# Kernel tuning notes

Hardware: AMD Instinct MI355X
Metric: run time of the kernel (lower is better)

## Reference

```python
import jax, jax.numpy as jnp
import numpy as np

N, E, D = 20000, 320000, 256
H, C = 8, 32  # heads, per-head channels (out_channels // heads)


def setup_inputs() -> dict:
    key = jax.random.key(0)
    ks = jax.random.split(key, 12)
    s = 1.0 / np.sqrt(D)
    return {
        "x": jax.random.normal(ks[0], (N, D), jnp.float32),
        "edge_index": jax.random.randint(ks[1], (2, E), 0, N, jnp.int64),
        "edge_attr": jax.random.normal(ks[2], (E, D), jnp.float32),
        "Wq": jax.random.normal(ks[3], (D, H * C), jnp.float32) * s,
        "bq": jnp.zeros((H * C,), jnp.float32),
        "Wk": jax.random.normal(ks[4], (D, H * C), jnp.float32) * s,
        "bk": jnp.zeros((H * C,), jnp.float32),
        "Wv": jax.random.normal(ks[5], (D, H * C), jnp.float32) * s,
        "bv": jnp.zeros((H * C,), jnp.float32),
        "We": jax.random.normal(ks[6], (D, H * C), jnp.float32) * s,  # lin_edge, no bias
        "Ws": jax.random.normal(ks[7], (D, H * C), jnp.float32) * s,  # lin_skip (root weight)
        "bs": jnp.zeros((H * C,), jnp.float32),
    }


def reference(x, edge_index, edge_attr, Wq, bq, Wk, bk, Wv, bv, We, Ws, bs):
    n = x.shape[0]
    src, dst = edge_index[0], edge_index[1]  # j (source), i (target)
    q = (x @ Wq + bq).reshape(n, H, C)
    k = (x @ Wk + bk).reshape(n, H, C)
    v = (x @ Wv + bv).reshape(n, H, C)
    e = (edge_attr @ We).reshape(-1, H, C)  # (E, H, C)

    kj = k[src] + e                      # key of source node + edge embedding
    alpha = jnp.einsum('ehc,ehc->eh', q[dst], kj) / jnp.sqrt(jnp.float32(C))
    # numerically-stable segment softmax over destination neighborhoods
    amax = jax.ops.segment_max(alpha, dst, num_segments=n)      # (N, H)
    ea = jnp.exp(alpha - amax[dst])                             # (E, H)
    denom = jax.ops.segment_sum(ea, dst, num_segments=n)        # (N, H)
    alpha = ea / (denom[dst] + 1e-16)

    msg = (v[src] + e) * alpha[:, :, None]                      # (E, H, C)
    out = jax.ops.segment_sum(msg, dst, num_segments=n)         # (N, H, C)
    out = out.reshape(n, H * C) + (x @ Ws + bs)                 # concat heads + skip
    return out
```

## Files before the change

### kernel.cpp

```cpp
#include <hip/hip_runtime.h>
#include <hip/hip_fp16.h>

#define N_NODES 20000
#define N_EDGES 320000
#define DIM 256

typedef _Float16 f16;
typedef unsigned int u32;
typedef f16 f16x8 __attribute__((ext_vector_type(8)));
typedef f16 f16x4 __attribute__((ext_vector_type(4)));
typedef float f32x4 __attribute__((ext_vector_type(4)));

#define GLL16(gsrc, ldst) __builtin_amdgcn_global_load_lds( \
    (const u32 __attribute__((address_space(1)))*)(gsrc),   \
    (u32 __attribute__((address_space(3)))*)(ldst), 16, 0, 0)

__global__ void prep_all(const float* __restrict__ Wq, const float* __restrict__ Wk,
                         const float* __restrict__ Wv, const float* __restrict__ Ws,
                         const float* __restrict__ We,
                         const float* __restrict__ bq, const float* __restrict__ bk,
                         const float* __restrict__ bv, const float* __restrict__ bs,
                         f16* __restrict__ wtbase, float* __restrict__ biasAll) {
    if (blockIdx.x < 1280) {
        int gid = blockIdx.x * 256 + threadIdx.x;
        int w = gid >> 16;
        int idx = gid & 65535;
        int k = idx >> 8, n = idx & 255;
        const float* W = (w == 0) ? Wq : (w == 1) ? Wk : (w == 2) ? Wv : (w == 3) ? Ws : We;
        wtbase[w * 65536 + n * 256 + k] = (f16)W[k * 256 + n];
    } else {
        int i = (blockIdx.x - 1280) * 256 + threadIdx.x;
        if (i < 1024) {
            int y = i >> 8, col = i & 255;
            const float* b = (y == 0) ? bq : (y == 1) ? bk : (y == 2) ? bv : bs;
            biasAll[i] = b[col];
        }
    }
}

template<int EDGE>
__global__ __launch_bounds__(256, 2) void gemm_v2(
    const float* __restrict__ A, const f16* __restrict__ WTbase,
    const float* __restrict__ biasAll,
    f16* __restrict__ outF16, float* __restrict__ outF32, int M)
{
    __shared__ __align__(16) char ldsB[2][16384];
    const int tid = threadIdx.x;
    const int wave = tid >> 6, lane = tid & 63;
    const int l16 = lane & 15, lg = lane >> 4;
    const int rowBase = blockIdx.x * 64 + (wave & 1) * 32;
    const int colBase = (wave >> 1) * 128;
    const int y = EDGE ? 0 : blockIdx.y;
    const f16* __restrict__ WT = WTbase + (EDGE ? 4 * 65536 : y * 65536);

    auto STAGE = [&](int b, int ks) {
#pragma unroll
        for (int i = 0; i < 4; ++i) {
            const int r = wave * 4 + i;
            const int n = r * 16 + (lane >> 2);
            const int kc = lane & 3;
            const f16* src = WT + n * 256 + ks * 32 + kc * 8;
            GLL16(src, &ldsB[b][r * 1024]);
        }
    };

    f32x4 a_lo[2], a_hi[2];
    auto LOADA = [&](int ks) {
#pragma unroll
        for (int m = 0; m < 2; ++m) {
            int row = rowBase + m * 16 + l16;
            if (row >= M) row = M - 1;
            const float* ap = A + (size_t)row * DIM + ks * 32 + lg * 8;
            a_lo[m] = *(const f32x4*)ap;
            a_hi[m] = *(const f32x4*)(ap + 4);
        }
    };

    f32x4 acc[2][8];
#pragma unroll
    for (int m = 0; m < 2; ++m)
#pragma unroll
        for (int c = 0; c < 8; ++c) acc[m][c] = (f32x4){0.f, 0.f, 0.f, 0.f};

    STAGE(0, 0);
    LOADA(0);

#pragma unroll
    for (int ks = 0; ks < 8; ++ks) {
        __syncthreads();
        if (ks < 7) STAGE((ks + 1) & 1, ks + 1);
        f16x8 afr[2];
#pragma unroll
        for (int m = 0; m < 2; ++m) {
#pragma unroll
            for (int j = 0; j < 4; ++j) {
                afr[m][j]     = (f16)a_lo[m][j];
                afr[m][4 + j] = (f16)a_hi[m][j];
            }
        }
        if (ks < 7) LOADA(ks + 1);
        const char* bbuf = ldsB[ks & 1];
#pragma unroll
        for (int ct = 0; ct < 8; ++ct) {
            f16x8 b = *(const f16x8*)(bbuf + (colBase + ct * 16 + l16) * 64 + lg * 16);
            acc[0][ct] = __builtin_amdgcn_mfma_f32_16x16x32_f16(afr[0], b, acc[0][ct], 0, 0, 0);
            acc[1][ct] = __builtin_amdgcn_mfma_f32_16x16x32_f16(afr[1], b, acc[1][ct], 0, 0, 0);
        }
    }

#pragma unroll
    for (int m = 0; m < 2; ++m) {
#pragma unroll
        for (int ct = 0; ct < 8; ++ct) {
            const int col = colBase + ct * 16 + l16;
            const float bv = EDGE ? 0.f : biasAll[y * 256 + col];
#pragma unroll
            for (int i = 0; i < 4; ++i) {
                const int row = rowBase + m * 16 + lg * 4 + i;
                if (row < M) {
                    const float val = acc[m][ct][i] + bv;
                    if (EDGE) {
                        outF16[(size_t)row * 256 + col] = (f16)val;
                    } else if (y < 3) {
                        (outF16 + (size_t)y * N_NODES * 256)[(size_t)row * 256 + col] = (f16)val;
                    } else {
                        outF32[(size_t)row * 256 + col] = val;
                    }
                }
            }
        }
    }
}

__global__ void count_deg(const int* __restrict__ dst, int* __restrict__ deg) {
    int e = blockIdx.x * blockDim.x + threadIdx.x;
    if (e < N_EDGES) atomicAdd(&deg[dst[e]], 1);
}

__global__ __launch_bounds__(1024) void scan_deg(const int* __restrict__ deg,
                                                 int* __restrict__ rowptr,
                                                 int* __restrict__ cursor) {
    __shared__ int part[1024];
    const int t = threadIdx.x;
    const int CH = (N_NODES + 1023) / 1024;
    const int base = t * CH;
    int s = 0;
    for (int i = 0; i < CH; ++i) { int n = base + i; if (n < N_NODES) s += deg[n]; }
    part[t] = s;
    __syncthreads();
    for (int off = 1; off < 1024; off <<= 1) {
        int v = (t >= off) ? part[t - off] : 0;
        __syncthreads();
        part[t] += v;
        __syncthreads();
    }
    int run = (t == 0) ? 0 : part[t - 1];
    for (int i = 0; i < CH; ++i) {
        int n = base + i;
        if (n < N_NODES) { int dn = deg[n]; rowptr[n] = run; cursor[n] = run; run += dn; }
    }
    if (t == 1023) rowptr[N_NODES] = part[1023];
}

__global__ void scatter_edges(const int* __restrict__ dst, int* __restrict__ cursor,
                              int* __restrict__ eids) {
    int e = blockIdx.x * blockDim.x + threadIdx.x;
    if (e < N_EDGES) { int p = atomicAdd(&cursor[dst[e]], 1); eids[p] = e; }
}

__global__ __launch_bounds__(256) void aggregate(
    const f16* __restrict__ qf, const f16* __restrict__ kf, const f16* __restrict__ vf,
    const f16* __restrict__ ef, const int* __restrict__ srcArr,
    const int* __restrict__ rowptr, const int* __restrict__ eids,
    float* __restrict__ out)
{
    const int wave = threadIdx.x >> 6;
    const int lane = threadIdx.x & 63;
    const int node = blockIdx.x * 4 + wave;
    if (node >= N_NODES) return;
    const int c0 = lane * 4;

    f32x4 qv;
    {
        f16x4 qh = *(const f16x4*)(qf + (size_t)node * 256 + c0);
        qv = (f32x4){(float)qh[0], (float)qh[1], (float)qh[2], (float)qh[3]};
    }
    float acc0 = 0.f, acc1 = 0.f, acc2 = 0.f, acc3 = 0.f, den = 0.f;
    const int beg = rowptr[node], end = rowptr[node + 1];
    for (int idx = beg; idx < end; ++idx) {
        const int eid = eids[idx];
        const int src = srcArr[eid];
        f16x4 eh = *(const f16x4*)(ef + (size_t)eid * 256 + c0);
        f16x4 kh = *(const f16x4*)(kf + (size_t)src * 256 + c0);
        f16x4 vh = *(const f16x4*)(vf + (size_t)src * 256 + c0);
        const float e0 = (float)eh[0], e1 = (float)eh[1], e2 = (float)eh[2], e3 = (float)eh[3];
        float d = qv[0] * ((float)kh[0] + e0) + qv[1] * ((float)kh[1] + e1)
                + qv[2] * ((float)kh[2] + e2) + qv[3] * ((float)kh[3] + e3);
        d += __shfl_xor(d, 1);
        d += __shfl_xor(d, 2);
        d += __shfl_xor(d, 4);
        const float ea = __expf(d * 0.1767766952966369f);
        den += ea;
        acc0 += ea * ((float)vh[0] + e0);
        acc1 += ea * ((float)vh[1] + e1);
        acc2 += ea * ((float)vh[2] + e2);
        acc3 += ea * ((float)vh[3] + e3);
    }
    const float inv = 1.0f / (den + 1e-16f);
    const size_t ob = (size_t)node * 256 + c0;
    f32x4 o = *(f32x4*)(out + ob);
    o[0] += acc0 * inv; o[1] += acc1 * inv; o[2] += acc2 * inv; o[3] += acc3 * inv;
    *(f32x4*)(out + ob) = o;
}

extern "C" void kernel_launch(void* const* d_in, const int* in_sizes, int n_in,
                              void* d_out, int out_size, void* d_ws, size_t ws_size,
                              hipStream_t stream) {
    const float* x   = (const float*)d_in[0];
    const int*   ei  = (const int*)d_in[1];
    const float* ea  = (const float*)d_in[2];
    const float* Wq  = (const float*)d_in[3];
    const float* bq  = (const float*)d_in[4];
    const float* Wk  = (const float*)d_in[5];
    const float* bk  = (const float*)d_in[6];
    const float* Wv  = (const float*)d_in[7];
    const float* bv  = (const float*)d_in[8];
    const float* We  = (const float*)d_in[9];
    const float* Ws  = (const float*)d_in[10];
    const float* bs  = (const float*)d_in[11];
    float* out = (float*)d_out;

    const int* srcArr = ei;
    const int* dstArr = ei + N_EDGES;

    char* w = (char*)d_ws;
    size_t off = 0;
    f16* wtbase = (f16*)(w + off); off += 5 * 65536 * 2;
    f16* qf = (f16*)(w + off); off += (size_t)N_NODES * 256 * 2;
    f16* kf = (f16*)(w + off); off += (size_t)N_NODES * 256 * 2;
    f16* vf = (f16*)(w + off); off += (size_t)N_NODES * 256 * 2;
    f16* ef = (f16*)(w + off); off += (size_t)N_EDGES * 256 * 2;
    int* deg    = (int*)(w + off); off += 80016;
    int* rowptr = (int*)(w + off); off += 80016;
    int* cursor = (int*)(w + off); off += 80016;
    int* eids   = (int*)(w + off); off += (size_t)N_EDGES * 4;
    float* biasAll = (float*)(w + off); off += 4 * 256 * 4;
    (void)ws_size; (void)n_in; (void)in_sizes; (void)out_size;

    prep_all<<<1284, 256, 0, stream>>>(Wq, Wk, Wv, Ws, We, bq, bk, bv, bs, wtbase, biasAll);

    hipMemsetAsync(deg, 0, N_NODES * 4, stream);
    count_deg<<<(N_EDGES + 255) / 256, 256, 0, stream>>>(dstArr, deg);
    scan_deg<<<1, 1024, 0, stream>>>(deg, rowptr, cursor);
    scatter_edges<<<(N_EDGES + 255) / 256, 256, 0, stream>>>(dstArr, cursor, eids);

    dim3 gnode((N_NODES + 63) / 64, 4);
    gemm_v2<0><<<gnode, 256, 0, stream>>>(x, wtbase, biasAll, qf, out, N_NODES);
    gemm_v2<1><<<N_EDGES / 64, 256, 0, stream>>>(ea, wtbase, nullptr, ef, nullptr, N_EDGES);

    aggregate<<<N_NODES / 4, 256, 0, stream>>>(qf, kf, vf, ef, srcArr, rowptr, eids, out);
}
```

Baseline: 391.8 us.

## Stage full weight matrix in LDS with swizzle and deepen A prefetch in GEMM

The GEMM block grows from 256 to 512 threads covering 128 rows. The whole 256x256 f16 weight matrix (128 KB) is loaded into LDS once per block with an XOR swizzle, which removes the per-k-step double-buffer syncs. The A operand is now prefetched three k-steps ahead instead of one, and the degree memset is replaced by a small zeroing kernel. The trade-off is heavy LDS use (128 KB per block), which limits blocks per CU and puts the whole weight load up front before any compute.

```diff
diff --git a/kernel.cpp b/kernel.cpp
--- a/kernel.cpp
+++ b/kernel.cpp
@@ -38,75 +38,83 @@
     }
 }
 
+__global__ void zero_deg(int* __restrict__ deg) {
+    int i = blockIdx.x * 256 + threadIdx.x;
+    if (i < N_NODES) deg[i] = 0;
+}
+
 template<int EDGE>
-__global__ __launch_bounds__(256, 2) void gemm_v2(
+__global__ __launch_bounds__(512, 2) void gemm_v3(
     const float* __restrict__ A, const f16* __restrict__ WTbase,
     const float* __restrict__ biasAll,
     f16* __restrict__ outF16, float* __restrict__ outF32, int M)
 {
-    __shared__ __align__(16) char ldsB[2][16384];
+    __shared__ __align__(16) char ldsB[131072];
     const int tid = threadIdx.x;
     const int wave = tid >> 6, lane = tid & 63;
     const int l16 = lane & 15, lg = lane >> 4;
-    const int rowBase = blockIdx.x * 64 + (wave & 1) * 32;
-    const int colBase = (wave >> 1) * 128;
-    const int y = EDGE ? 0 : blockIdx.y;
-    const f16* __restrict__ WT = WTbase + (EDGE ? 4 * 65536 : y * 65536);
-
-    auto STAGE = [&](int b, int ks) {
-#pragma unroll
-        for (int i = 0; i < 4; ++i) {
-            const int r = wave * 4 + i;
-            const int n = r * 16 + (lane >> 2);
-            const int kc = lane & 3;
-            const f16* src = WT + n * 256 + ks * 32 + kc * 8;
-            GLL16(src, &ldsB[b][r * 1024]);
-        }
-    };
-
-    f32x4 a_lo[2], a_hi[2];
-    auto LOADA = [&](int ks) {
+    const int rowBase = blockIdx.x * 128 + (wave & 3) * 32;
+    const int colBase = (wave >> 2) * 128;
+    const int y = EDGE ? 4 : blockIdx.y;
+    const f16* __restrict__ WT = WTbase + y * 65536;
+
+    {
+        const int nrel = lane >> 2;
+        const int kc = (lane & 3) ^ ((lane >> 3) & 3);
+        const f16* srcBase = WT + wave * 32 + kc * 8;
+#pragma unroll
+        for (int r = 0; r < 16; ++r) {
+            const f16* src = srcBase + (size_t)(r * 16 + nrel) * 256;
+            GLL16(src, &ldsB[wave * 16384 + r * 1024]);
+        }
+    }
+
+    f32x4 alo[3][2], ahi[3][2];
+#define LOADA(ks_, s_) do {                                                   \
+    _Pragma("unroll")                                                         \
+    for (int m_ = 0; m_ < 2; ++m_) {                                          \
+        int row_ = rowBase + m_ * 16 + l16;                                   \
+        if (row_ >= M) row_ = M - 1;                                          \
+        const float* ap_ = A + (size_t)row_ * DIM + (ks_) * 32 + lg * 8;      \
+        alo[s_][m_] = *(const f32x4*)ap_;                                     \
+        ahi[s_][m_] = *(const f32x4*)(ap_ + 4);                               \
+    } } while (0)
+
+    LOADA(0, 0); LOADA(1, 1); LOADA(2, 2);
+
+    f32x4 acc[2][8];
+#pragma unroll
+    for (int m = 0; m < 2; ++m)
+#pragma unroll
+        for (int c = 0; c < 8; ++c) acc[m][c] = (f32x4){0.f, 0.f, 0.f, 0.f};
+
+    const int swzRead = (lg ^ ((l16 >> 1) & 3)) * 16;
+
+    __syncthreads();
+
+#pragma unroll
+    for (int ks = 0; ks < 8; ++ks) {
+        const int slot = ks % 3;
+        f16x8 afr[2];
 #pragma unroll
         for (int m = 0; m < 2; ++m) {
-            int row = rowBase + m * 16 + l16;
-            if (row >= M) row = M - 1;
-            const float* ap = A + (size_t)row * DIM + ks * 32 + lg * 8;
-            a_lo[m] = *(const f32x4*)ap;
-            a_hi[m] = *(const f32x4*)(ap + 4);
-        }
-    };
-
-    f32x4 acc[2][8];
-#pragma unroll
-    for (int m = 0; m < 2; ++m)
-#pragma unroll
-        for (int c = 0; c < 8; ++c) acc[m][c] = (f32x4){0.f, 0.f, 0.f, 0.f};
-
-    STAGE(0, 0);
-    LOADA(0);
-
-#pragma unroll
-    for (int ks = 0; ks < 8; ++ks) {
-        __syncthreads();
-        if (ks < 7) STAGE((ks + 1) & 1, ks + 1);
-        f16x8 afr[2];
-#pragma unroll
-        for (int m = 0; m < 2; ++m) {
 #pragma unroll
             for (int j = 0; j < 4; ++j) {
-                afr[m][j]     = (f16)a_lo[m][j];
-                afr[m][4 + j] = (f16)a_hi[m][j];
+                afr[m][j]     = (f16)alo[slot][m][j];
+                afr[m][4 + j] = (f16)ahi[slot][m][j];
             }
         }
-        if (ks < 7) LOADA(ks + 1);
-        const char* bbuf = ldsB[ks & 1];
+        if (ks < 5) LOADA(ks + 3, slot);
+        const char* bbuf = ldsB + ks * 16384;
 #pragma unroll
         for (int ct = 0; ct < 8; ++ct) {
-            f16x8 b = *(const f16x8*)(bbuf + (colBase + ct * 16 + l16) * 64 + lg * 16);
+            const int n = colBase + ct * 16 + l16;
+            f16x8 b = *(const f16x8*)(bbuf + n * 64 + swzRead);
             acc[0][ct] = __builtin_amdgcn_mfma_f32_16x16x32_f16(afr[0], b, acc[0][ct], 0, 0, 0);
             acc[1][ct] = __builtin_amdgcn_mfma_f32_16x16x32_f16(afr[1], b, acc[1][ct], 0, 0, 0);
         }
     }
+#undef LOADA
 
 #pragma unroll
     for (int m = 0; m < 2; ++m) {
@@ -249,14 +257,14 @@
 
     prep_all<<<1284, 256, 0, stream>>>(Wq, Wk, Wv, Ws, We, bq, bk, bv, bs, wtbase, biasAll);
 
-    hipMemsetAsync(deg, 0, N_NODES * 4, stream);
+    zero_deg<<<(N_NODES + 255) / 256, 256, 0, stream>>>(deg);
     count_deg<<<(N_EDGES + 255) / 256, 256, 0, stream>>>(dstArr, deg);
     scan_deg<<<1, 1024, 0, stream>>>(deg, rowptr, cursor);
     scatter_edges<<<(N_EDGES + 255) / 256, 256, 0, stream>>>(dstArr, cursor, eids);
 
-    dim3 gnode((N_NODES + 63) / 64, 4);
-    gemm_v2<0><<<gnode, 256, 0, stream>>>(x, wtbase, biasAll, qf, out, N_NODES);
-    gemm_v2<1><<<N_EDGES / 64, 256, 0, stream>>>(ea, wtbase, nullptr, ef, nullptr, N_EDGES);
+    dim3 gnode((N_NODES + 127) / 128, 4);
+    gemm_v3<0><<<gnode, 512, 0, stream>>>(x, wtbase, biasAll, qf, out, N_NODES);
+    gemm_v3<1><<<N_EDGES / 128, 512, 0, stream>>>(ea, wtbase, nullptr, ef, nullptr, N_EDGES);
 
     aggregate<<<N_NODES / 4, 256, 0, stream>>>(qf, kf, vf, ef, srcArr, rowptr, eids, out);
 }
```

Result: no change. 385.7 us (-1.5%).

## Write edge projections in CSR order and restructure GEMM with full-K LDS staging

Applied to the files above, without the earlier changes.

The edge GEMM now gathers edge_attr rows through the CSR permutation (eids), so edge embeddings are stored in destination-sorted order. The aggregate kernel can then read e and a pre-permuted src array contiguously instead of taking two dependent indirections per edge. The GEMM is rewritten to 512 threads with 128-row by 128-column tiles. It loads the whole K dimension of A into registers and a swizzled full-K B tile into LDS in one stage, which removes the per-k-step double-buffer syncs. Other changes: the deg memset is folded into prep_all, and the aggregate loop is unrolled by two. The cost is a random gather on edge_attr reads and higher register and LDS pressure in the GEMM.

```diff
diff --git a/kernel.cpp b/kernel.cpp
--- a/kernel.cpp
+++ b/kernel.cpp
@@ -20,7 +20,8 @@
                          const float* __restrict__ We,
                          const float* __restrict__ bq, const float* __restrict__ bk,
                          const float* __restrict__ bv, const float* __restrict__ bs,
-                         f16* __restrict__ wtbase, float* __restrict__ biasAll) {
+                         f16* __restrict__ wtbase, float* __restrict__ biasAll,
+                         int* __restrict__ deg) {
     if (blockIdx.x < 1280) {
         int gid = blockIdx.x * 256 + threadIdx.x;
         int w = gid >> 16;
@@ -28,104 +29,96 @@
         int k = idx >> 8, n = idx & 255;
         const float* W = (w == 0) ? Wq : (w == 1) ? Wk : (w == 2) ? Wv : (w == 3) ? Ws : We;
         wtbase[w * 65536 + n * 256 + k] = (f16)W[k * 256 + n];
+    } else if (blockIdx.x < 1284) {
+        int i = (blockIdx.x - 1280) * 256 + threadIdx.x;
+        int y = i >> 8, col = i & 255;
+        const float* b = (y == 0) ? bq : (y == 1) ? bk : (y == 2) ? bv : bs;
+        biasAll[i] = b[col];
     } else {
-        int i = (blockIdx.x - 1280) * 256 + threadIdx.x;
-        if (i < 1024) {
-            int y = i >> 8, col = i & 255;
-            const float* b = (y == 0) ? bq : (y == 1) ? bk : (y == 2) ? bv : bs;
-            biasAll[i] = b[col];
-        }
+        int i = (blockIdx.x - 1284) * 256 + threadIdx.x;
+        if (i < N_NODES) deg[i] = 0;
     }
 }
 
 template<int EDGE>
-__global__ __launch_bounds__(256, 2) void gemm_v2(
+__global__ __launch_bounds__(512, 4) void gemm_v4(
     const float* __restrict__ A, const f16* __restrict__ WTbase,
-    const float* __restrict__ biasAll,
+    const float* __restrict__ biasAll, const int* __restrict__ eids,
     f16* __restrict__ outF16, float* __restrict__ outF32, int M)
 {
-    __shared__ __align__(16) char ldsB[2][16384];
+    __shared__ __align__(16) char lds[65536];
     const int tid = threadIdx.x;
     const int wave = tid >> 6, lane = tid & 63;
     const int l16 = lane & 15, lg = lane >> 4;
-    const int rowBase = blockIdx.x * 64 + (wave & 1) * 32;
-    const int colBase = (wave >> 1) * 128;
-    const int y = EDGE ? 0 : blockIdx.y;
-    const f16* __restrict__ WT = WTbase + (EDGE ? 4 * 65536 : y * 65536);
-
-    auto STAGE = [&](int b, int ks) {
+    const int y = blockIdx.y;
+    const int outSel  = EDGE ? 4 : (y >> 1);
+    const int colHalf = EDGE ? y : (y & 1);
+    const f16* __restrict__ WT = WTbase + outSel * 65536 + colHalf * 128 * 256;
+    const int rowBase = blockIdx.x * 128 + wave * 16;
+
+    const int slot = rowBase + l16;
+    int arow;
+    if (EDGE) arow = eids[slot];
+    else      arow = (slot < M) ? slot : M - 1;
+    const float* ap = A + (size_t)arow * DIM;
+    f32x4 lo[8], hi[8];
+#pragma unroll
+    for (int ks = 0; ks < 8; ++ks) {
+        lo[ks] = *(const f32x4*)(ap + ks * 32 + lg * 8);
+        hi[ks] = *(const f32x4*)(ap + ks * 32 + lg * 8 + 4);
+    }
+
+    {
+        const int p = lane & 31;
+#pragma unroll
+        for (int r = 0; r < 8; ++r) {
+            const int nrel = wave * 16 + r * 2 + (lane >> 5);
+            const f16* src = WT + nrel * 256 + (p ^ (nrel & 31)) * 8;
+            GLL16(src, &lds[(wave * 16 + r * 2) * 512]);
+        }
+    }
+
+    f16x8 afr[8];
+#pragma unroll
+    for (int ks = 0; ks < 8; ++ks) {
+#pragma unroll
+        for (int j = 0; j < 4; ++j) {
+            afr[ks][j]     = (f16)lo[ks][j];
+            afr[ks][4 + j] = (f16)hi[ks][j];
+        }
+    }
+
+    f32x4 acc[8];
+#pragma unroll
+    for (int c = 0; c < 8; ++c) acc[c] = (f32x4){0.f, 0.f, 0.f, 0.f};
+
+    __syncthreads();
+
+#pragma unroll
+    for (int ks = 0; ks < 8; ++ks) {
+#pragma unroll
+        for (int ct = 0; ct < 8; ++ct) {
+            const int nrel = ct * 16 + l16;
+            f16x8 b = *(const f16x8*)(lds + nrel * 512 + (((ks * 4 + lg) ^ (nrel & 31)) * 16));
+            acc[ct] = __builtin_amdgcn_mfma_f32_16x16x32_f16(afr[ks], b, acc[ct], 0, 0, 0);
+        }
+    }
+
+#pragma unroll
+    for (int ct = 0; ct < 8; ++ct) {
+        const int col = colHalf * 128 + ct * 16 + l16;
+        const float bv = EDGE ? 0.f : biasAll[outSel * 256 + col];
 #pragma unroll
         for (int i = 0; i < 4; ++i) {
-            const int r = wave * 4 + i;
-            const int n = r * 16 + (lane >> 2);
-            const int kc = lane & 3;
-            const f16* src = WT + n * 256 + ks * 32 + kc * 8;
-            GLL16(src, &ldsB[b][r * 1024]);
-        }
-    };
-
-    f32x4 a_lo[2], a_hi[2];
-    auto LOADA = [&](int ks) {
-#pragma unroll
-        for (int m = 0; m < 2; ++m) {
-            int row = rowBase + m * 16 + l16;
-            if (row >= M) row = M - 1;
-            const float* ap = A + (size_t)row * DIM + ks * 32 + lg * 8;
-            a_lo[m] = *(const f32x4*)ap;
-            a_hi[m] = *(const f32x4*)(ap + 4);
-        }
-    };
-
-    f32x4 acc[2][8];
-#pragma unroll
-    for (int m = 0; m < 2; ++m)
-#pragma unroll
-        for (int c = 0; c < 8; ++c) acc[m][c] = (f32x4){0.f, 0.f, 0.f, 0.f};
-
-    STAGE(0, 0);
-    LOADA(0);
-
-#pragma unroll
-    for (int ks = 0; ks < 8; ++ks) {
-        __syncthreads();
-        if (ks < 7) STAGE((ks + 1) & 1, ks + 1);
-        f16x8 afr[2];
-#pragma unroll
-        for (int m = 0; m < 2; ++m) {
-#pragma unroll
-            for (int j = 0; j < 4; ++j) {
-                afr[m][j]     = (f16)a_lo[m][j];
-                afr[m][4 + j] = (f16)a_hi[m][j];
-            }
-        }
-        if (ks < 7) LOADA(ks + 1);
-        const char* bbuf = ldsB[ks & 1];
-#pragma unroll
-        for (int ct = 0; ct < 8; ++ct) {
-            f16x8 b = *(const f16x8*)(bbuf + (colBase + ct * 16 + l16) * 64 + lg * 16);
-            acc[0][ct] = __builtin_amdgcn_mfma_f32_16x16x32_f16(afr[0], b, acc[0][ct], 0, 0, 0);
-            acc[1][ct] = __builtin_amdgcn_mfma_f32_16x16x32_f16(afr[1], b, acc[1][ct], 0, 0, 0);
-        }
-    }
-
-#pragma unroll
-    for (int m = 0; m < 2; ++m) {
-#pragma unroll
-        for (int ct = 0; ct < 8; ++ct) {
-            const int col = colBase + ct * 16 + l16;
-            const float bv = EDGE ? 0.f : biasAll[y * 256 + col];
-#pragma unroll
-            for (int i = 0; i < 4; ++i) {
-                const int row = rowBase + m * 16 + lg * 4 + i;
-                if (row < M) {
-                    const float val = acc[m][ct][i] + bv;
-                    if (EDGE) {
-                        outF16[(size_t)row * 256 + col] = (f16)val;
-                    } else if (y < 3) {
-                        (outF16 + (size_t)y * N_NODES * 256)[(size_t)row * 256 + col] = (f16)val;
-                    } else {
-                        outF32[(size_t)row * 256 + col] = val;
-                    }
+            const int row = rowBase + lg * 4 + i;
+            if (EDGE || row < M) {
+                const float val = acc[ct][i] + bv;
+                if (EDGE) {
+                    outF16[(size_t)row * 256 + col] = (f16)val;
+                } else if (outSel < 3) {
+                    (outF16 + (size_t)outSel * N_NODES * 256)[(size_t)row * 256 + col] = (f16)val;
+                } else {
+                    outF32[(size_t)row * 256 + col] = val;
                 }
             }
         }
@@ -162,17 +155,21 @@
     if (t == 1023) rowptr[N_NODES] = part[1023];
 }
 
-__global__ void scatter_edges(const int* __restrict__ dst, int* __restrict__ cursor,
-                              int* __restrict__ eids) {
+__global__ void scatter_edges(const int* __restrict__ src, const int* __restrict__ dst,
+                              int* __restrict__ cursor,
+                              int* __restrict__ eids, int* __restrict__ srcs) {
     int e = blockIdx.x * blockDim.x + threadIdx.x;
-    if (e < N_EDGES) { int p = atomicAdd(&cursor[dst[e]], 1); eids[p] = e; }
+    if (e < N_EDGES) {
+        int p = atomicAdd(&cursor[dst[e]], 1);
+        eids[p] = e;
+        srcs[p] = src[e];
+    }
 }
 
 __global__ __launch_bounds__(256) void aggregate(
     const f16* __restrict__ qf, const f16* __restrict__ kf, const f16* __restrict__ vf,
-    const f16* __restrict__ ef, const int* __restrict__ srcArr,
-    const int* __restrict__ rowptr, const int* __restrict__ eids,
-    float* __restrict__ out)
+    const f16* __restrict__ ef, const int* __restrict__ srcs,
+    const int* __restrict__ rowptr, float* __restrict__ out)
 {
     const int wave = threadIdx.x >> 6;
     const int lane = threadIdx.x & 63;
@@ -187,25 +184,32 @@
     }
     float acc0 = 0.f, acc1 = 0.f, acc2 = 0.f, acc3 = 0.f, den = 0.f;
     const int beg = rowptr[node], end = rowptr[node + 1];
-    for (int idx = beg; idx < end; ++idx) {
-        const int eid = eids[idx];
-        const int src = srcArr[eid];
-        f16x4 eh = *(const f16x4*)(ef + (size_t)eid * 256 + c0);
-        f16x4 kh = *(const f16x4*)(kf + (size_t)src * 256 + c0);
-        f16x4 vh = *(const f16x4*)(vf + (size_t)src * 256 + c0);
-        const float e0 = (float)eh[0], e1 = (float)eh[1], e2 = (float)eh[2], e3 = (float)eh[3];
-        float d = qv[0] * ((float)kh[0] + e0) + qv[1] * ((float)kh[1] + e1)
-                + qv[2] * ((float)kh[2] + e2) + qv[3] * ((float)kh[3] + e3);
-        d += __shfl_xor(d, 1);
-        d += __shfl_xor(d, 2);
-        d += __shfl_xor(d, 4);
-        const float ea = __expf(d * 0.1767766952966369f);
-        den += ea;
-        acc0 += ea * ((float)vh[0] + e0);
-        acc1 += ea * ((float)vh[1] + e1);
-        acc2 += ea * ((float)vh[2] + e2);
-        acc3 += ea * ((float)vh[3] + e3);
-    }
+
+#define BODY(ii) {                                                              \
+        const int src = srcs[ii];                                               \
+        f16x4 eh = *(const f16x4*)(ef + (size_t)(ii) * 256 + c0);               \
+        f16x4 kh = *(const f16x4*)(kf + (size_t)src * 256 + c0);                \
+        f16x4 vh = *(const f16x4*)(vf + (size_t)src * 256 + c0);                \
+        const float e0 = (float)eh[0], e1 = (float)eh[1];                       \
+        const float e2 = (float)eh[2], e3 = (float)eh[3];                       \
+        float d = qv[0] * ((float)kh[0] + e0) + qv[1] * ((float)kh[1] + e1)     \
+                + qv[2] * ((float)kh[2] + e2) + qv[3] * ((float)kh[3] + e3);    \
+        d += __shfl_xor(d, 1);                                                  \
+        d += __shfl_xor(d, 2);                                                  \
+        d += __shfl_xor(d, 4);                                                  \
+        const float w_ = __expf(d * 0.1767766952966369f);                       \
+        den += w_;                                                              \
+        acc0 += w_ * ((float)vh[0] + e0);                                       \
+        acc1 += w_ * ((float)vh[1] + e1);                                       \
+        acc2 += w_ * ((float)vh[2] + e2);                                       \
+        acc3 += w_ * ((float)vh[3] + e3);                                       \
+    }
+
+    int idx = beg;
+    for (; idx + 1 < end; idx += 2) { BODY(idx); BODY(idx + 1); }
+    if (idx < end) BODY(idx);
+#undef BODY
+
     const float inv = 1.0f / (den + 1e-16f);
     const size_t ob = (size_t)node * 256 + c0;
     f32x4 o = *(f32x4*)(out + ob);
@@ -244,19 +248,21 @@
     int* rowptr = (int*)(w + off); off += 80016;
     int* cursor = (int*)(w + off); off += 80016;
     int* eids   = (int*)(w + off); off += (size_t)N_EDGES * 4;
+    int* srcs   = (int*)(w + off); off += (size_t)N_EDGES * 4;
     float* biasAll = (float*)(w + off); off += 4 * 256 * 4;
     (void)ws_size; (void)n_in; (void)in_sizes; (void)out_size;
 
-    prep_all<<<1284, 256, 0, stream>>>(Wq, Wk, Wv, Ws, We, bq, bk, bv, bs, wtbase, biasAll);
-
-    hipMemsetAsync(deg, 0, N_NODES * 4, stream);
+    prep_all<<<1284 + (N_NODES + 255) / 256, 256, 0, stream>>>(
+        Wq, Wk, Wv, Ws, We, bq, bk, bv, bs, wtbase, biasAll, deg);
+
     count_deg<<<(N_EDGES + 255) / 256, 256, 0, stream>>>(dstArr, deg);
     scan_deg<<<1, 1024, 0, stream>>>(deg, rowptr, cursor);
-    scatter_edges<<<(N_EDGES + 255) / 256, 256, 0, stream>>>(dstArr, cursor, eids);
-
-    dim3 gnode((N_NODES + 63) / 64, 4);
-    gemm_v2<0><<<gnode, 256, 0, stream>>>(x, wtbase, biasAll, qf, out, N_NODES);
-    gemm_v2<1><<<N_EDGES / 64, 256, 0, stream>>>(ea, wtbase, nullptr, ef, nullptr, N_EDGES);
-
-    aggregate<<<N_NODES / 4, 256, 0, stream>>>(qf, kf, vf, ef, srcArr, rowptr, eids, out);
-}
+    scatter_edges<<<(N_EDGES + 255) / 256, 256, 0, stream>>>(srcArr, dstArr, cursor, eids, srcs);
+
+    dim3 gnode((N_NODES + 127) / 128, 8);
+    gemm_v4<0><<<gnode, 512, 0, stream>>>(x, wtbase, biasAll, nullptr, qf, out, N_NODES);
+    dim3 gedge(N_EDGES / 128, 2);
+    gemm_v4<1><<<gedge, 512, 0, stream>>>(ea, wtbase, nullptr, eids, ef, nullptr, N_EDGES);
+
+    aggregate<<<N_NODES / 4, 256, 0, stream>>>(qf, kf, vf, ef, srcs, rowptr, out);
+}
```

After: 389.6 us. Within noise of the previous version (-0.6%).
